# Kernel optimization log

Hardware: AMD Instinct MI355X
Metric: run time of the kernel (lower is better)

Reference implementation:

```python
import jax, jax.numpy as jnp
import numpy as np

B, N1, N2, D = 2, 512, 512, 128


def setup_inputs() -> dict:
    key = jax.random.key(0)
    ks = jax.random.split(key, 7)
    return {
        "x0": jax.random.normal(ks[0], (B, N1, D), dtype=jnp.float32),
        "x": jax.random.normal(ks[1], (B, N1, D), dtype=jnp.float32),
        "y": jax.random.normal(ks[2], (B, N2, D), dtype=jnp.float32),
        "W1": jax.random.normal(ks[3], (3 * D, D), dtype=jnp.float32) * (1.0 / np.sqrt(3 * D)),
        "b1": jax.random.normal(ks[4], (D,), dtype=jnp.float32) * 0.02,
        "W2": jax.random.normal(ks[5], (D, 1), dtype=jnp.float32) * (1.0 / np.sqrt(D)),
        "b2": jax.random.normal(ks[6], (1,), dtype=jnp.float32) * 0.02,
    }


def reference(x0, x, y, W1, b1, W2, b2):
    # linear1(concat([x0, x, y], -1)) == x0 @ W1[:D] + x @ W1[D:2D] + y @ W1[2D:] + b1
    d = x.shape[-1]
    Wa, Wb, Wc = W1[:d], W1[d:2 * d], W1[2 * d:]
    # small GEMMs on the un-expanded operands, then broadcast-add over the pair grid
    hx = jnp.einsum('bnd,de->bne', x0, Wa) + jnp.einsum('bnd,de->bne', x, Wb)  # [b, n1, d]
    hy = jnp.einsum('bmd,de->bme', y, Wc)                                      # [b, n2, d]
    h = hx[:, :, None, :] + hy[:, None, :, :] + b1                             # [b, n1, n2, d]
    h = jax.nn.gelu(h, approximate=False)                                      # torch nn.GELU default (erf)
    o = jnp.einsum('bnme,eo->bnmo', h, W2) + b2                                # [b, n1, n2, 1]
    return o[..., 0]                                                           # [b, n1, n2]
```

## Files before the change

kernel.cpp:

```cpp
#include <hip/hip_runtime.h>

#define BB 2
#define NN1 512
#define NN2 512
#define DD 128
#define TS 16
#define SXPAD 132

__device__ __forceinline__ float gelu_fast(float s) {
    const float C1 = -2.3021181584f;
    const float C2 = -0.1029532929f;
    float t = s * s;
    float u = s * __builtin_fmaf(C2, t, C1);
    float e = __builtin_amdgcn_exp2f(u);
    float r = __builtin_amdgcn_rcpf(1.0f + e);
    return s * r;
}

#define PR 8
__global__ __launch_bounds__(256) void proj_kernel(
    const float* __restrict__ x0, const float* __restrict__ x,
    const float* __restrict__ y,  const float* __restrict__ W1,
    const float* __restrict__ b1, float* __restrict__ hx, float* __restrict__ hy) {
    const int e = threadIdx.x & (DD - 1);
    const int g = threadIdx.x >> 7;
    const int nxb = (BB * NN1) / PR;
    const float* Wa = W1;
    const float* Wb = W1 + DD * DD;
    const float* Wc = W1 + 2 * DD * DD;

    if (blockIdx.x < nxb) {
        const int row0 = blockIdx.x * PR + g * (PR / 2);
        float acc0 = b1[e], acc1 = b1[e], acc2 = b1[e], acc3 = b1[e];
        #pragma unroll 4
        for (int d = 0; d < DD; ++d) {
            const float wa = Wa[d * DD + e];
            const float wb = Wb[d * DD + e];
            acc0 += x0[(row0 + 0) * DD + d] * wa + x[(row0 + 0) * DD + d] * wb;
            acc1 += x0[(row0 + 1) * DD + d] * wa + x[(row0 + 1) * DD + d] * wb;
            acc2 += x0[(row0 + 2) * DD + d] * wa + x[(row0 + 2) * DD + d] * wb;
            acc3 += x0[(row0 + 3) * DD + d] * wa + x[(row0 + 3) * DD + d] * wb;
        }
        hx[(row0 + 0) * DD + e] = acc0;
        hx[(row0 + 1) * DD + e] = acc1;
        hx[(row0 + 2) * DD + e] = acc2;
        hx[(row0 + 3) * DD + e] = acc3;
    } else {
        const int row0 = (blockIdx.x - nxb) * PR + g * (PR / 2);
        float acc0 = 0.f, acc1 = 0.f, acc2 = 0.f, acc3 = 0.f;
        #pragma unroll 4
        for (int d = 0; d < DD; ++d) {
            const float wc = Wc[d * DD + e];
            acc0 += y[(row0 + 0) * DD + d] * wc;
            acc1 += y[(row0 + 1) * DD + d] * wc;
            acc2 += y[(row0 + 2) * DD + d] * wc;
            acc3 += y[(row0 + 3) * DD + d] * wc;
        }
        hy[(row0 + 0) * DD + e] = acc0;
        hy[(row0 + 1) * DD + e] = acc1;
        hy[(row0 + 2) * DD + e] = acc2;
        hy[(row0 + 3) * DD + e] = acc3;
    }
}

__global__ __launch_bounds__(256) void cross_kernel(
    const float* __restrict__ hx, const float* __restrict__ hy,
    const float* __restrict__ W2, const float* __restrict__ b2,
    float* __restrict__ out) {
    __shared__ float sx[TS][SXPAD];
    __shared__ float sy[TS][SXPAD];
    __shared__ float sw[DD];

    const int b  = blockIdx.z;
    const int n0 = blockIdx.y * TS;
    const int m0 = blockIdx.x * TS;
    const int tid = threadIdx.x;

    for (int i = tid; i < TS * (DD / 4); i += 256) {
        const int r  = i >> 5;
        const int c4 = i & 31;
        *(float4*)&sx[r][c4 * 4] =
            *(const float4*)&hx[((b * NN1) + n0 + r) * DD + c4 * 4];
        *(float4*)&sy[r][c4 * 4] =
            *(const float4*)&hy[((b * NN2) + m0 + r) * DD + c4 * 4];
    }
    if (tid < DD) sw[tid] = W2[tid];
    __syncthreads();

    const int tn = tid >> 4;
    const int tm = tid & 15;

    float acc = b2[0];
    #pragma unroll 8
    for (int e4 = 0; e4 < DD / 4; ++e4) {
        const float4 a = *(const float4*)&sx[tn][e4 * 4];
        const float4 c = *(const float4*)&sy[tm][e4 * 4];
        const float4 w = *(const float4*)&sw[e4 * 4];
        acc += gelu_fast(a.x + c.x) * w.x;
        acc += gelu_fast(a.y + c.y) * w.y;
        acc += gelu_fast(a.z + c.z) * w.z;
        acc += gelu_fast(a.w + c.w) * w.w;
    }
    out[((b * NN1) + n0 + tn) * NN2 + m0 + tm] = acc;
}

extern "C" void kernel_launch(void* const* d_in, const int* in_sizes, int n_in,
                              void* d_out, int out_size, void* d_ws, size_t ws_size,
                              hipStream_t stream) {
    const float* x0 = (const float*)d_in[0];
    const float* x  = (const float*)d_in[1];
    const float* y  = (const float*)d_in[2];
    const float* W1 = (const float*)d_in[3];
    const float* b1 = (const float*)d_in[4];
    const float* W2 = (const float*)d_in[5];
    const float* b2 = (const float*)d_in[6];
    float* out = (float*)d_out;

    float* hx = (float*)d_ws;
    float* hy = hx + (size_t)BB * NN1 * DD;

    const int nblocks = (BB * NN1) / PR + (BB * NN2) / PR;
    proj_kernel<<<nblocks, 256, 0, stream>>>(x0, x, y, W1, b1, hx, hy);
    cross_kernel<<<dim3(NN2 / TS, NN1 / TS, BB), 256, 0, stream>>>(hx, hy, W2, b2, out);
}
```

Baseline: 42.75 us.

## Compute 2x2 output register tile per thread with 32x32 block tiles

Each block now covers a 32x32 tile of the pair grid instead of 16x16, and each thread computes a 2x2 output micro-tile. Every shared-memory load of hx, hy and W2 is reused across four GELU evaluations, which cuts LDS traffic per output. The grid has a quarter as many blocks (512), and the extra accumulators raise register pressure and may lower occupancy. The kernel is dominated by GELU math, so the benefit depends on how much the LDS reads were limiting it.

```diff
diff --git a/kernel.cpp b/kernel.cpp
--- a/kernel.cpp
+++ b/kernel.cpp
@@ -4,7 +4,7 @@
 #define NN1 512
 #define NN2 512
 #define DD 128
-#define TS 16
+#define TS 32
 #define SXPAD 132
 
 __device__ __forceinline__ float gelu_fast(float s) {
@@ -87,21 +87,45 @@
     if (tid < DD) sw[tid] = W2[tid];
     __syncthreads();
 
-    const int tn = tid >> 4;
-    const int tm = tid & 15;
+    const int tn = (tid >> 4) * 2;
+    const int tm = (tid & 15) * 2;
 
-    float acc = b2[0];
-    #pragma unroll 8
+    float acc00 = 0.f, acc01 = 0.f, acc10 = 0.f, acc11 = 0.f;
+
+    #pragma unroll 4
     for (int e4 = 0; e4 < DD / 4; ++e4) {
-        const float4 a = *(const float4*)&sx[tn][e4 * 4];
-        const float4 c = *(const float4*)&sy[tm][e4 * 4];
-        const float4 w = *(const float4*)&sw[e4 * 4];
-        acc += gelu_fast(a.x + c.x) * w.x;
-        acc += gelu_fast(a.y + c.y) * w.y;
-        acc += gelu_fast(a.z + c.z) * w.z;
-        acc += gelu_fast(a.w + c.w) * w.w;
+        const float4 a0 = *(const float4*)&sx[tn][e4 * 4];
+        const float4 a1 = *(const float4*)&sx[tn + 1][e4 * 4];
+        const float4 c0 = *(const float4*)&sy[tm][e4 * 4];
+        const float4 c1 = *(const float4*)&sy[tm + 1][e4 * 4];
+        const float4 w  = *(const float4*)&sw[e4 * 4];
+
+        acc00 += gelu_fast(a0.x + c0.x) * w.x;
+        acc01 += gelu_fast(a0.x + c1.x) * w.x;
+        acc10 += gelu_fast(a1.x + c0.x) * w.x;
+        acc11 += gelu_fast(a1.x + c1.x) * w.x;
+
+        acc00 += gelu_fast(a0.y + c0.y) * w.y;
+        acc01 += gelu_fast(a0.y + c1.y) * w.y;
+        acc10 += gelu_fast(a1.y + c0.y) * w.y;
+        acc11 += gelu_fast(a1.y + c1.y) * w.y;
+
+        acc00 += gelu_fast(a0.z + c0.z) * w.z;
+        acc01 += gelu_fast(a0.z + c1.z) * w.z;
+        acc10 += gelu_fast(a1.z + c0.z) * w.z;
+        acc11 += gelu_fast(a1.z + c1.z) * w.z;
+
+        acc00 += gelu_fast(a0.w + c0.w) * w.w;
+        acc01 += gelu_fast(a0.w + c1.w) * w.w;
+        acc10 += gelu_fast(a1.w + c0.w) * w.w;
+        acc11 += gelu_fast(a1.w + c1.w) * w.w;
     }
-    out[((b * NN1) + n0 + tn) * NN2 + m0 + tm] = acc;
+
+    const float bias = b2[0];
+    float* o0 = &out[((size_t)(b * NN1) + n0 + tn) * NN2 + m0 + tm];
+    float* o1 = o0 + NN2;
+    *(float2*)o0 = make_float2(acc00 + bias, acc01 + bias);
+    *(float2*)o1 = make_float2(acc10 + bias, acc11 + bias);
 }
 
 extern "C" void kernel_launch(void* const* d_in, const int* in_sizes, int n_in,
```

After: 41.68 us. 1.03x faster.
